# Optimization experiments

Hardware: AMD Instinct MI355X
Metric: run time of the kernel (lower is better)

Reference implementation:

```python
import jax, jax.numpy as jnp
import numpy as np

B, S, IN_DIM = 8, 4096, 1024
H, D = 16, 64          # num_heads, head_dim (attention_dim = H*D = 1024)
OUT_DIM = 1024
EPS = 1e-6
HI = jax.lax.Precision.HIGHEST


def setup_inputs() -> dict:
    key = jax.random.key(0)
    ks = jax.random.split(key, 9)
    sx = 1.0 / np.sqrt(IN_DIM)
    so = 1.0 / np.sqrt(H * D)
    return {
        "x":  jax.random.normal(ks[0], (B, S, IN_DIM), jnp.float32),
        "wq": jax.random.normal(ks[1], (IN_DIM, H, D), jnp.float32) * sx,
        "bq": jnp.zeros((H, D), jnp.float32),
        "wk": jax.random.normal(ks[2], (IN_DIM, H, D), jnp.float32) * sx,
        "bk": jnp.zeros((H, D), jnp.float32),
        "wv": jax.random.normal(ks[3], (IN_DIM, H, D), jnp.float32) * sx,
        "bv": jnp.zeros((H, D), jnp.float32),
        "wo": jax.random.normal(ks[4], (H, D, OUT_DIM), jnp.float32) * so,
        "bo": jnp.zeros((OUT_DIM,), jnp.float32),
    }


def _feature_map(t):
    return jax.nn.elu(t) + 1.0


def reference(x, wq, bq, wk, bk, wv, bv, wo, bo):
    # QKV projections: [B,S,IN] x [IN,H,D] -> [B,S,H,D]
    q = jnp.einsum('bsi,ihd->bshd', x, wq) + bq
    k = jnp.einsum('bsi,ihd->bshd', x, wk) + bk
    v = jnp.einsum('bsi,ihd->bshd', x, wv) + bv

    Q = _feature_map(q)
    K = _feature_map(k)

    # Faithful to source: KV is an elementwise K*V reduced over seq -> [B,H,D]
    KV = jnp.einsum('bshd,bshd->bhd', K, v, precision=HI)
    Ksum = jnp.sum(K, axis=1)                      # [B,H,D]
    Z = 1.0 / (Q * Ksum[:, None, :, :] + EPS)      # [B,S,H,D]
    attn = Q * KV[:, None, :, :] * Z               # [B,S,H,D]

    # output projection contracts heads and head_dim
    out = jnp.einsum('bshd,hdo->bso', attn, wo) + bo
    return jax.nn.gelu(out)  # flax default gelu is approximate=True
```

## Files before the change

### kernel.cpp

```cpp
#include <hip/hip_runtime.h>


#define SEQ   4096
#define MROWS 32768
#define KDIM  1024
#define HD    1024
#define T32   32

typedef __bf16 bf16x8 __attribute__((ext_vector_type(8)));
typedef float floatx4 __attribute__((ext_vector_type(4)));

__device__ __forceinline__ unsigned short f2bf(float f) {
    unsigned int u = __float_as_uint(f);
    u += 0x7fffu + ((u >> 16) & 1u);
    return (unsigned short)(u >> 16);
}
__device__ __forceinline__ void cvt8(const float* __restrict__ p, unsigned short* d) {
    const float4 a = *(const float4*)p;
    const float4 b = *(const float4*)(p + 4);
    d[0] = f2bf(a.x); d[1] = f2bf(a.y); d[2] = f2bf(a.z); d[3] = f2bf(a.w);
    d[4] = f2bf(b.x); d[5] = f2bf(b.y); d[6] = f2bf(b.z); d[7] = f2bf(b.w);
}

typedef const __attribute__((address_space(1))) unsigned int* gas_t;
typedef __attribute__((address_space(3))) unsigned int* las_t;
__device__ __forceinline__ void async16(const void* g, void* l) {
    __builtin_amdgcn_global_load_lds((gas_t)g, (las_t)l, 16, 0, 0);
}

__global__ __launch_bounds__(256)
void cvt_x(const float* __restrict__ x, unsigned short* __restrict__ xb)
{
    const size_t p = ((size_t)blockIdx.x * 256 + threadIdx.x) * 8;
    union { uint4 u; unsigned short s[8]; } o;
    cvt8(x + p, o.s);
    *(uint4*)(xb + p) = o.u;
}

__global__ __launch_bounds__(256)
void transpose_w(const float* __restrict__ wk, const float* __restrict__ wv,
                 unsigned short* __restrict__ wkT, unsigned short* __restrict__ wvT)
{
    __shared__ alignas(16) unsigned short Ts[64][72];
    const float* W = blockIdx.z ? wv : wk;
    unsigned short* WT = blockIdx.z ? wvT : wkT;
    const int k0 = blockIdx.x * 64, n0 = blockIdx.y * 64;
    const int t = threadIdx.x;
    const int r4 = (t >> 4) * 4, c4 = (t & 15) * 4;
#pragma unroll
    for (int i = 0; i < 4; i++) {
        const float4 f = *(const float4*)(W + (size_t)(k0 + r4 + i) * HD + n0 + c4);
        Ts[c4 + 0][r4 + i] = f2bf(f.x);
        Ts[c4 + 1][r4 + i] = f2bf(f.y);
        Ts[c4 + 2][r4 + i] = f2bf(f.z);
        Ts[c4 + 3][r4 + i] = f2bf(f.w);
    }
    __syncthreads();
    const int rr = t >> 3, cc = (t & 7) * 8;
#pragma unroll
    for (int h = 0; h < 2; h++)
        *(uint4*)(WT + (size_t)(n0 + rr + h * 32) * KDIM + k0 + cc) =
            *(const uint4*)&Ts[rr + h * 32][cc];
}

__global__ __launch_bounds__(512, 2)
void kv_gemm_fast(const unsigned short* __restrict__ xb,
                  const unsigned short* __restrict__ wkT,
                  const unsigned short* __restrict__ wvT,
                  const float* __restrict__ bk, const float* __restrict__ bv,
                  float2* __restrict__ KVZ)
{
    __shared__ alignas(16) unsigned short As[4][256 * 32];
    __shared__ alignas(16) unsigned short Bs[4][256 * 32];

    const int t = threadIdx.x;

    const int id = blockIdx.x;
    const int xcd = id & 7, o = id >> 3;
    const int mtile = xcd * 16 + (o >> 3);
    const int ntile = o & 7;
    const int m0 = mtile * 256;
    const int n0 = ntile * 128;
    const int b  = m0 >> 12;

    const int w = t >> 6, lane = t & 63;
    const int wm = w >> 1, wn = w & 1;
    const int lrow = lane & 15, quad = lane >> 4;

    const int usw = quad ^ ((lrow >> 1) & 3);

    const int srow  = t >> 2;
    const int usrc  = (t & 3) ^ ((t >> 3) & 3);
    const unsigned short* gA0 = xb  + (size_t)(m0 + srow) * KDIM + usrc * 8;
    const unsigned short* gA1 = gA0 + (size_t)128 * KDIM;
    const unsigned short* gBk = wkT + (size_t)(n0 + srow) * KDIM + usrc * 8;
    const unsigned short* gBv = wvT + (size_t)(n0 + srow) * KDIM + usrc * 8;

#define STAGE(c, tk) do {                                                     \
        const int ko_ = (tk) * 32;                                            \
        async16(gA0 + ko_, &As[c][(0 * 512 + t) * 8]);                        \
        async16(gA1 + ko_, &As[c][(1 * 512 + t) * 8]);                        \
        async16(gBk + ko_, &Bs[c][(0 * 512 + t) * 8]);                        \
        async16(gBv + ko_, &Bs[c][(1 * 512 + t) * 8]);                        \
    } while (0)

    bf16x8 afA[4], bKA[4], bVA[4];
    bf16x8 afB[4], bKB[4], bVB[4];

#define LOADSET(af_, bK_, bV_, c) do {                                        \
        _Pragma("unroll")                                                     \
        for (int mi = 0; mi < 4; ++mi)                                        \
            af_[mi] = *(const bf16x8*)&As[c][(wm * 64 + mi * 16 + lrow) * 32 + usw * 8]; \
        _Pragma("unroll")                                                     \
        for (int ni = 0; ni < 4; ++ni) {                                      \
            const int br_ = wn * 64 + ni * 16 + lrow;                         \
            bK_[ni] = *(const bf16x8*)&Bs[c][ br_        * 32 + usw * 8];     \
            bV_[ni] = *(const bf16x8*)&Bs[c][(br_ + 128) * 32 + usw * 8];     \
        }                                                                     \
    } while (0)

#define MFMASET(af_, bK_, bV_) do {                                           \
        __builtin_amdgcn_s_setprio(1);                                        \
        _Pragma("unroll")                                                     \
        for (int mi = 0; mi < 4; ++mi)                                        \
            _Pragma("unroll")                                                 \
            for (int ni = 0; ni < 4; ++ni) {                                  \
                accK[mi][ni] = __builtin_amdgcn_mfma_f32_16x16x32_bf16(       \
                    af_[mi], bK_[ni], accK[mi][ni], 0, 0, 0);                 \
                accV[mi][ni] = __builtin_amdgcn_mfma_f32_16x16x32_bf16(       \
                    af_[mi], bV_[ni], accV[mi][ni], 0, 0, 0);                 \
            }                                                                 \
        __builtin_amdgcn_s_setprio(0);                                        \
    } while (0)

#define WAIT8 asm volatile("s_waitcnt vmcnt(8)" ::: "memory")
#define BAR   __builtin_amdgcn_s_barrier()

    floatx4 accK[4][4], accV[4][4];
#pragma unroll
    for (int i = 0; i < 4; i++)
#pragma unroll
        for (int j = 0; j < 4; j++) {
            accK[i][j] = (floatx4){0.f, 0.f, 0.f, 0.f};
            accV[i][j] = (floatx4){0.f, 0.f, 0.f, 0.f};
        }

    STAGE(0, 0);
    STAGE(1, 1);
    STAGE(2, 2);
    WAIT8;
    BAR;
    LOADSET(afA, bKA, bVA, 0);

    for (int it = 0; it < 7; ++it) {
        const int tk = it * 4;
        STAGE(3, tk + 3); WAIT8; BAR; LOADSET(afB, bKB, bVB, 1); MFMASET(afA, bKA, bVA);
        STAGE(0, tk + 4); WAIT8; BAR; LOADSET(afA, bKA, bVA, 2); MFMASET(afB, bKB, bVB);
        STAGE(1, tk + 5); WAIT8; BAR; LOADSET(afB, bKB, bVB, 3); MFMASET(afA, bKA, bVA);
        STAGE(2, tk + 6); WAIT8; BAR; LOADSET(afA, bKA, bVA, 0); MFMASET(afB, bKB, bVB);
    }

    STAGE(3, 31); WAIT8; BAR;
    LOADSET(afB, bKB, bVB, 1); MFMASET(afA, bKA, bVA);
    asm volatile("s_waitcnt vmcnt(4)" ::: "memory"); BAR;
    LOADSET(afA, bKA, bVA, 2); MFMASET(afB, bKB, bVB);
    asm volatile("s_waitcnt vmcnt(0)" ::: "memory"); BAR;
    LOADSET(afB, bKB, bVB, 3); MFMASET(afA, bKA, bVA);
    MFMASET(afB, bKB, bVB);

#undef STAGE
#undef LOADSET
#undef MFMASET
#undef WAIT8
#undef BAR

#pragma unroll
    for (int ni = 0; ni < 4; ++ni) {
        const int colw = n0 + wn * 64 + ni * 16 + lrow;
        const float bkf = bk[colw];
        const float bvf = bv[colw];
        float pKV = 0.f, pK = 0.f;
#pragma unroll
        for (int mi = 0; mi < 4; ++mi) {
#pragma unroll
            for (int r = 0; r < 4; ++r) {
                const float kk = accK[mi][ni][r] + bkf;
                const float K  = (kk > 0.f) ? (kk + 1.f) : __expf(kk);
                const float vv = accV[mi][ni][r] + bvf;
                pKV += K * vv;
                pK  += K;
            }
        }
        pKV += __shfl_xor(pKV, 16, 64);
        pKV += __shfl_xor(pKV, 32, 64);
        pK  += __shfl_xor(pK, 16, 64);
        pK  += __shfl_xor(pK, 32, 64);
        if (quad == 0) {
            atomicAdd(&KVZ[b * HD + colw].x, pKV);
            atomicAdd(&KVZ[b * HD + colw].y, pK);
        }
    }
}

__global__ __launch_bounds__(256)
void kv_gemm(const float* __restrict__ x,
             const float* __restrict__ wk, const float* __restrict__ bk,
             const float* __restrict__ wv, const float* __restrict__ bv,
             float2* __restrict__ KVZ)
{
    __shared__ alignas(16) unsigned short As [128][40];
    __shared__ alignas(16) unsigned short BsK[128][40];
    __shared__ alignas(16) unsigned short BsV[128][40];

    const int t = threadIdx.x;
    const int n0 = blockIdx.x * 128;
    const int m0 = blockIdx.y * 128;
    const int b  = m0 >> 12;

    const int wave = t >> 6, lane = t & 63;
    const int wm = wave >> 1, wn = wave & 1;
    const int lrow = lane & 15, quad = lane >> 4;

    floatx4 accK[4][4], accV[4][4];
#pragma unroll
    for (int i = 0; i < 4; i++)
#pragma unroll
        for (int j = 0; j < 4; j++) {
            accK[i][j] = (floatx4){0.f, 0.f, 0.f, 0.f};
            accV[i][j] = (floatx4){0.f, 0.f, 0.f, 0.f};
        }

    const int arow0 = t >> 2, akc = (t & 3) * 8;
    const int bk0 = t >> 4, bnc = (t & 15) * 8;

    for (int k0 = 0; k0 < KDIM; k0 += 32) {
        __syncthreads();
        {
            union { uint4 u; unsigned short s[8]; } ua, ub;
            cvt8(x + (size_t)(m0 + arow0) * KDIM + k0 + akc, ua.s);
            cvt8(x + (size_t)(m0 + arow0 + 64) * KDIM + k0 + akc, ub.s);
            *(uint4*)&As[arow0][akc] = ua.u;
            *(uint4*)&As[arow0 + 64][akc] = ub.u;
        }
        {
            unsigned short k0s[8], k1s[8], v0s[8], v1s[8];
            cvt8(wk + (size_t)(k0 + bk0) * HD + n0 + bnc, k0s);
            cvt8(wk + (size_t)(k0 + bk0 + 16) * HD + n0 + bnc, k1s);
            cvt8(wv + (size_t)(k0 + bk0) * HD + n0 + bnc, v0s);
            cvt8(wv + (size_t)(k0 + bk0 + 16) * HD + n0 + bnc, v1s);
#pragma unroll
            for (int j = 0; j < 8; j++) {
                BsK[bnc + j][bk0]      = k0s[j];
                BsK[bnc + j][bk0 + 16] = k1s[j];
                BsV[bnc + j][bk0]      = v0s[j];
                BsV[bnc + j][bk0 + 16] = v1s[j];
            }
        }
        __syncthreads();

        bf16x8 af[4], bfK[4], bfV[4];
#pragma unroll
        for (int mi = 0; mi < 4; mi++)
            af[mi] = *(const bf16x8*)&As[wm * 64 + mi * 16 + lrow][quad * 8];
#pragma unroll
        for (int ni = 0; ni < 4; ni++) {
            bfK[ni] = *(const bf16x8*)&BsK[wn * 64 + ni * 16 + lrow][quad * 8];
            bfV[ni] = *(const bf16x8*)&BsV[wn * 64 + ni * 16 + lrow][quad * 8];
        }
#pragma unroll
        for (int mi = 0; mi < 4; mi++)
#pragma unroll
            for (int ni = 0; ni < 4; ni++) {
                accK[mi][ni] = __builtin_amdgcn_mfma_f32_16x16x32_bf16(
                    af[mi], bfK[ni], accK[mi][ni], 0, 0, 0);
                accV[mi][ni] = __builtin_amdgcn_mfma_f32_16x16x32_bf16(
                    af[mi], bfV[ni], accV[mi][ni], 0, 0, 0);
            }
    }

#pragma unroll
    for (int ni = 0; ni < 4; ni++) {
        const int colw = n0 + wn * 64 + ni * 16 + lrow;
        const float bkf = bk[colw];
        const float bvf = bv[colw];
        float pKV = 0.f, pK = 0.f;
#pragma unroll
        for (int mi = 0; mi < 4; mi++) {
#pragma unroll
            for (int r = 0; r < 4; r++) {
                const float kk = accK[mi][ni][r] + bkf;
                const float K  = (kk > 0.f) ? (kk + 1.f) : __expf(kk);
                const float vv = accV[mi][ni][r] + bvf;
                pKV += K * vv;
                pK  += K;
            }
        }
        pKV += __shfl_xor(pKV, 16, 64);
        pKV += __shfl_xor(pKV, 32, 64);
        pK  += __shfl_xor(pK, 16, 64);
        pK  += __shfl_xor(pK, 32, 64);
        if (quad == 0) {
            atomicAdd(&KVZ[b * HD + colw].x, pKV);
            atomicAdd(&KVZ[b * HD + colw].y, pK);
        }
    }
}

__global__ __launch_bounds__(256)
void rowgemm_bcast(const float2* __restrict__ KVZ,
                   const float* __restrict__ wo, const float* __restrict__ bo,
                   float* __restrict__ out)
{
    __shared__ float a[1024];
    __shared__ float red[4][64];
    __shared__ float sval[64];
    const int t = threadIdx.x;
    const int b = blockIdx.x;
    const int o0 = blockIdx.y * 64;
    const int s0 = blockIdx.z * 512;

    for (int c = t; c < 1024; c += 256) {
        const float2 z = KVZ[b * HD + c];
        a[c] = z.x / z.y;
    }
    __syncthreads();

    const int cs = t >> 6, oi = t & 63;
    float p = 0.f;
    const int cbeg = cs * 256;
    for (int c = cbeg; c < cbeg + 256; ++c)
        p += a[c] * wo[(size_t)c * HD + o0 + oi];
    red[cs][oi] = p;
    __syncthreads();

    if (t < 64) {
        float v = red[0][t] + red[1][t] + red[2][t] + red[3][t] + bo[o0 + t];
        sval[t] = 0.5f * v *
            (1.f + tanhf(0.7978845608028654f * (v + 0.044715f * v * v * v)));
    }
    __syncthreads();

    const float4 sv4 = *(const float4*)&sval[(t & 15) * 4];
    for (int r = t >> 4; r < 512; r += 16)
        *(float4*)&out[((size_t)(b * SEQ + s0 + r)) * HD + o0 + (t & 15) * 4] = sv4;
}

__global__ __launch_bounds__(256)
void rowgemm(const float2* __restrict__ KVZ,
             const float* __restrict__ wo, const float* __restrict__ bo,
             float* __restrict__ rowf)
{
    __shared__ float a[1024];
    __shared__ float red[4][64];
    const int t = threadIdx.x;
    const int b = blockIdx.x;
    const int o0 = blockIdx.y * 64;

    for (int c = t; c < 1024; c += 256) {
        const float2 z = KVZ[b * HD + c];
        a[c] = z.x / z.y;
    }
    __syncthreads();

    const int cs = t >> 6, oi = t & 63;
    float p = 0.f;
    const int cbeg = cs * 256;
    for (int c = cbeg; c < cbeg + 256; ++c)
        p += a[c] * wo[(size_t)c * HD + o0 + oi];
    red[cs][oi] = p;
    __syncthreads();

    if (t < 64) {
        float v = red[0][t] + red[1][t] + red[2][t] + red[3][t] + bo[o0 + t];
        const float g = 0.5f * v *
            (1.f + tanhf(0.7978845608028654f * (v + 0.044715f * v * v * v)));
        rowf[b * HD + o0 + t] = g;
    }
}

__global__ __launch_bounds__(256)
void broadcast_rows(const float* __restrict__ rowf, float* __restrict__ out)
{
    const size_t idx = (size_t)blockIdx.x * 256 + threadIdx.x;
    const size_t p = idx * 4;
    const int row = (int)(p >> 10);
    const int b = row >> 12;
    const int col = (int)(p & 1023);
    *(float4*)(out + p) = *(const float4*)(rowf + b * HD + col);
}

extern "C" void kernel_launch(void* const* d_in, const int* in_sizes, int n_in,
                              void* d_out, int out_size, void* d_ws, size_t ws_size,
                              hipStream_t stream)
{
    const float* x  = (const float*)d_in[0];
    const float* wk = (const float*)d_in[3];
    const float* bk = (const float*)d_in[4];
    const float* wv = (const float*)d_in[5];
    const float* bv = (const float*)d_in[6];
    const float* wo = (const float*)d_in[7];
    const float* bo = (const float*)d_in[8];
    float* out = (float*)d_out;

    const size_t NEED = (size_t)72 * 1024 * 1024;
    if (ws_size >= NEED) {
        unsigned short* xb  = (unsigned short*)d_ws;
        unsigned short* wkT = (unsigned short*)((char*)d_ws + (67u << 20));
        unsigned short* wvT = (unsigned short*)((char*)d_ws + (69u << 20));
        float2* KVZ = (float2*)((char*)d_ws + (71u << 20));

        hipMemsetAsync(KVZ, 0, 8 * HD * sizeof(float2), stream);
        cvt_x<<<dim3(MROWS * KDIM / 8 / 256), 256, 0, stream>>>(x, xb);
        transpose_w<<<dim3(16, 16, 2), 256, 0, stream>>>(wk, wv, wkT, wvT);
        kv_gemm_fast<<<dim3(1024), 512, 0, stream>>>(xb, wkT, wvT, bk, bv, KVZ);
        rowgemm_bcast<<<dim3(8, 16, 8), 256, 0, stream>>>(KVZ, wo, bo, out);
    } else {
        float2* KVZ = (float2*)d_ws;
        float* rowf = (float*)((char*)d_ws + 65536);
        hipMemsetAsync(KVZ, 0, 8 * HD * sizeof(float2), stream);
        kv_gemm<<<dim3(8, 256), 256, 0, stream>>>(x, wk, bk, wv, bv, KVZ);
        rowgemm<<<dim3(8, 16), 256, 0, stream>>>(KVZ, wo, bo, rowf);
        broadcast_rows<<<dim3((MROWS * HD / 4) / 256), 256, 0, stream>>>(rowf, out);
    }
}
```

Measured before the change: 405.0 us.

## Load B operands directly to registers and merge prep kernels into one launch

The GEMM kernel stops staging the Wk/Wv tiles through LDS and loads them from global memory straight into registers, prefetched one k-tile ahead. Only the x tile still goes through the four-stage async LDS pipeline, and the wait and barrier schedule is rewritten around it. The x conversion and weight transpose kernels become one launch, and the launch bound drops from two blocks per CU to one. This removes B-side LDS traffic and one kernel launch. In exchange it adds uncoalesced global loads per wave, duplicated B reads across wm waves, and register pressure.

```diff
diff --git a/kernel.cpp b/kernel.cpp
--- a/kernel.cpp
+++ b/kernel.cpp
@@ -5,7 +5,6 @@
 #define MROWS 32768
 #define KDIM  1024
 #define HD    1024
-#define T32   32
 
 typedef __bf16 bf16x8 __attribute__((ext_vector_type(8)));
 typedef float floatx4 __attribute__((ext_vector_type(4)));
@@ -29,23 +28,23 @@
 }
 
 __global__ __launch_bounds__(256)
-void cvt_x(const float* __restrict__ x, unsigned short* __restrict__ xb)
-{
-    const size_t p = ((size_t)blockIdx.x * 256 + threadIdx.x) * 8;
-    union { uint4 u; unsigned short s[8]; } o;
-    cvt8(x + p, o.s);
-    *(uint4*)(xb + p) = o.u;
-}
-
-__global__ __launch_bounds__(256)
-void transpose_w(const float* __restrict__ wk, const float* __restrict__ wv,
-                 unsigned short* __restrict__ wkT, unsigned short* __restrict__ wvT)
+void prep(const float* __restrict__ x, unsigned short* __restrict__ xb,
+          const float* __restrict__ wk, const float* __restrict__ wv,
+          unsigned short* __restrict__ wkT, unsigned short* __restrict__ wvT)
 {
     __shared__ alignas(16) unsigned short Ts[64][72];
-    const float* W = blockIdx.z ? wv : wk;
-    unsigned short* WT = blockIdx.z ? wvT : wkT;
-    const int k0 = blockIdx.x * 64, n0 = blockIdx.y * 64;
     const int t = threadIdx.x;
+    if (blockIdx.x < 16384) {
+        const size_t p = ((size_t)blockIdx.x * 256 + t) * 8;
+        union { uint4 u; unsigned short s[8]; } o;
+        cvt8(x + p, o.s);
+        *(uint4*)(xb + p) = o.u;
+        return;
+    }
+    const int bid = blockIdx.x - 16384;
+    const float* W = (bid >> 8) ? wv : wk;
+    unsigned short* WT = (bid >> 8) ? wvT : wkT;
+    const int k0 = (bid & 15) * 64, n0 = ((bid >> 4) & 15) * 64;
     const int r4 = (t >> 4) * 4, c4 = (t & 15) * 4;
 #pragma unroll
     for (int i = 0; i < 4; i++) {
@@ -63,7 +62,7 @@
             *(const uint4*)&Ts[rr + h * 32][cc];
 }
 
-__global__ __launch_bounds__(512, 2)
+__global__ __launch_bounds__(512, 1)
 void kv_gemm_fast(const unsigned short* __restrict__ xb,
                   const unsigned short* __restrict__ wkT,
                   const unsigned short* __restrict__ wvT,
@@ -71,7 +70,6 @@
                   float2* __restrict__ KVZ)
 {
     __shared__ alignas(16) unsigned short As[4][256 * 32];
-    __shared__ alignas(16) unsigned short Bs[4][256 * 32];
 
     const int t = threadIdx.x;
 
@@ -91,50 +89,52 @@
 
     const int srow  = t >> 2;
     const int usrc  = (t & 3) ^ ((t >> 3) & 3);
-    const unsigned short* gA0 = xb  + (size_t)(m0 + srow) * KDIM + usrc * 8;
+    const unsigned short* gA0 = xb + (size_t)(m0 + srow) * KDIM + usrc * 8;
     const unsigned short* gA1 = gA0 + (size_t)128 * KDIM;
-    const unsigned short* gBk = wkT + (size_t)(n0 + srow) * KDIM + usrc * 8;
-    const unsigned short* gBv = wvT + (size_t)(n0 + srow) * KDIM + usrc * 8;
-
-#define STAGE(c, tk) do {                                                     \
+
+    const unsigned short* gBk = wkT + (size_t)(n0 + wn * 64 + lrow) * KDIM + quad * 8;
+    const unsigned short* gBv = wvT + (size_t)(n0 + wn * 64 + lrow) * KDIM + quad * 8;
+
+#define STAGE_A(c, tk) do {                                                   \
         const int ko_ = (tk) * 32;                                            \
-        async16(gA0 + ko_, &As[c][(0 * 512 + t) * 8]);                        \
-        async16(gA1 + ko_, &As[c][(1 * 512 + t) * 8]);                        \
-        async16(gBk + ko_, &Bs[c][(0 * 512 + t) * 8]);                        \
-        async16(gBv + ko_, &Bs[c][(1 * 512 + t) * 8]);                        \
+        async16(gA0 + ko_, &As[c][ t        * 8]);                            \
+        async16(gA1 + ko_, &As[c][(512 + t) * 8]);                            \
     } while (0)
 
-    bf16x8 afA[4], bKA[4], bVA[4];
-    bf16x8 afB[4], bKB[4], bVB[4];
-
-#define LOADSET(af_, bK_, bV_, c) do {                                        \
+    bf16x8 PK[4], PV[4], QK[4], QV[4];
+
+#define LOADB(K_, V_, tk) do {                                                \
+        _Pragma("unroll")                                                     \
+        for (int ni = 0; ni < 4; ++ni) {                                      \
+            K_[ni] = *(const bf16x8*)(gBk + ni * 16 * KDIM + (tk) * 32);      \
+            V_[ni] = *(const bf16x8*)(gBv + ni * 16 * KDIM + (tk) * 32);      \
+        }                                                                     \
+    } while (0)
+
+#define TILE_BODY(tk, CK, CV, NK, NV, DOLB, DOST, NWAIT) do {                 \
+        const unsigned short* A_ = As[(tk) & 3];                              \
+        bf16x8 af[4];                                                         \
         _Pragma("unroll")                                                     \
         for (int mi = 0; mi < 4; ++mi)                                        \
-            af_[mi] = *(const bf16x8*)&As[c][(wm * 64 + mi * 16 + lrow) * 32 + usw * 8]; \
-        _Pragma("unroll")                                                     \
-        for (int ni = 0; ni < 4; ++ni) {                                      \
-            const int br_ = wn * 64 + ni * 16 + lrow;                         \
-            bK_[ni] = *(const bf16x8*)&Bs[c][ br_        * 32 + usw * 8];     \
-            bV_[ni] = *(const bf16x8*)&Bs[c][(br_ + 128) * 32 + usw * 8];     \
-        }                                                                     \
-    } while (0)
-
-#define MFMASET(af_, bK_, bV_) do {                                           \
+            af[mi] = *(const bf16x8*)&A_[(wm * 64 + mi * 16 + lrow) * 32 + usw * 8]; \
+        if (DOLB) LOADB(NK, NV, (tk) + 1);                                    \
+        if (DOST) STAGE_A(((tk) + 3) & 3, (tk) + 3);                          \
         __builtin_amdgcn_s_setprio(1);                                        \
         _Pragma("unroll")                                                     \
         for (int mi = 0; mi < 4; ++mi)                                        \
             _Pragma("unroll")                                                 \
             for (int ni = 0; ni < 4; ++ni) {                                  \
                 accK[mi][ni] = __builtin_amdgcn_mfma_f32_16x16x32_bf16(       \
-                    af_[mi], bK_[ni], accK[mi][ni], 0, 0, 0);                 \
+                    af[mi], CK[ni], accK[mi][ni], 0, 0, 0);                   \
                 accV[mi][ni] = __builtin_amdgcn_mfma_f32_16x16x32_bf16(       \
-                    af_[mi], bV_[ni], accV[mi][ni], 0, 0, 0);                 \
+                    af[mi], CV[ni], accV[mi][ni], 0, 0, 0);                   \
             }                                                                 \
         __builtin_amdgcn_s_setprio(0);                                        \
+        if (NWAIT == 12) asm volatile("s_waitcnt vmcnt(12)" ::: "memory");    \
+        else if (NWAIT == 10) asm volatile("s_waitcnt vmcnt(10)" ::: "memory");\
+        else if (NWAIT == 8)  asm volatile("s_waitcnt vmcnt(8)"  ::: "memory");\
+        if (NWAIT >= 0) __builtin_amdgcn_s_barrier();                         \
     } while (0)
-
-#define WAIT8 asm volatile("s_waitcnt vmcnt(8)" ::: "memory")
-#define BAR   __builtin_amdgcn_s_barrier()
 
     floatx4 accK[4][4], accV[4][4];
 #pragma unroll
@@ -145,34 +145,26 @@
             accV[i][j] = (floatx4){0.f, 0.f, 0.f, 0.f};
         }
 
-    STAGE(0, 0);
-    STAGE(1, 1);
-    STAGE(2, 2);
-    WAIT8;
-    BAR;
-    LOADSET(afA, bKA, bVA, 0);
-
-    for (int it = 0; it < 7; ++it) {
-        const int tk = it * 4;
-        STAGE(3, tk + 3); WAIT8; BAR; LOADSET(afB, bKB, bVB, 1); MFMASET(afA, bKA, bVA);
-        STAGE(0, tk + 4); WAIT8; BAR; LOADSET(afA, bKA, bVA, 2); MFMASET(afB, bKB, bVB);
-        STAGE(1, tk + 5); WAIT8; BAR; LOADSET(afB, bKB, bVB, 3); MFMASET(afA, bKA, bVA);
-        STAGE(2, tk + 6); WAIT8; BAR; LOADSET(afA, bKA, bVA, 0); MFMASET(afB, bKB, bVB);
-    }
-
-    STAGE(3, 31); WAIT8; BAR;
-    LOADSET(afB, bKB, bVB, 1); MFMASET(afA, bKA, bVA);
-    asm volatile("s_waitcnt vmcnt(4)" ::: "memory"); BAR;
-    LOADSET(afA, bKA, bVA, 2); MFMASET(afB, bKB, bVB);
-    asm volatile("s_waitcnt vmcnt(0)" ::: "memory"); BAR;
-    LOADSET(afB, bKB, bVB, 3); MFMASET(afA, bKA, bVA);
-    MFMASET(afB, bKB, bVB);
-
-#undef STAGE
-#undef LOADSET
-#undef MFMASET
-#undef WAIT8
-#undef BAR
+    STAGE_A(0, 0);
+    STAGE_A(1, 1);
+    STAGE_A(2, 2);
+    LOADB(PK, PV, 0);
+    asm volatile("s_waitcnt vmcnt(12)" ::: "memory");
+    __builtin_amdgcn_s_barrier();
+
+    for (int it = 0; it < 14; ++it) {
+        const int tk = it * 2;
+        TILE_BODY(tk,     PK, PV, QK, QV, 1, 1, 12);
+        TILE_BODY(tk + 1, QK, QV, PK, PV, 1, 1, 12);
+    }
+    TILE_BODY(28, PK, PV, QK, QV, 1, 1, 12);
+    TILE_BODY(29, QK, QV, PK, PV, 1, 0, 10);
+    TILE_BODY(30, PK, PV, QK, QV, 1, 0, 8);
+    TILE_BODY(31, QK, QV, PK, PV, 0, 0, -1);
+
+#undef STAGE_A
+#undef LOADB
+#undef TILE_BODY
 
 #pragma unroll
     for (int ni = 0; ni < 4; ++ni) {
@@ -410,8 +402,7 @@
         float2* KVZ = (float2*)((char*)d_ws + (71u << 20));
 
         hipMemsetAsync(KVZ, 0, 8 * HD * sizeof(float2), stream);
-        cvt_x<<<dim3(MROWS * KDIM / 8 / 256), 256, 0, stream>>>(x, xb);
-        transpose_w<<<dim3(16, 16, 2), 256, 0, stream>>>(wk, wv, wkT, wvT);
+        prep<<<dim3(16384 + 512), 256, 0, stream>>>(x, xb, wk, wv, wkT, wvT);
         kv_gemm_fast<<<dim3(1024), 512, 0, stream>>>(xb, wkT, wvT, bk, bv, KVZ);
         rowgemm_bcast<<<dim3(8, 16, 8), 256, 0, stream>>>(KVZ, wo, bo, out);
     } else {
```

Measured after the change: 560.2 us. +38.3%, slower.
